# Kernel tuning notes

Measured on AMD Instinct MI355X. Metric: run time of the kernel, lower is better.

The kernel has to match this reference:

```python
import jax, jax.numpy as jnp
import numpy as np

DT = 0.1       # time separation between grid points (forward dt arg default)
UT = 0.1       # stationary-mode time constant
K_IN, K_OUT, K_STATE = 8, 4, 128
PRE_LEN, FWD_LEN, BATCH = 64, 128, 4096


def setup_inputs() -> dict:
    key = jax.random.key(0)
    ks = jax.random.split(key, 16)
    H = K_STATE
    s = 0.05  # small init keeps the 128-step integration numerically tame
    d = {}
    d['pre_x'] = jax.random.normal(ks[0], (PRE_LEN, BATCH, K_IN), jnp.float32)
    d['pre_y'] = jax.random.normal(ks[1], (PRE_LEN, BATCH, K_OUT), jnp.float32)
    d['forward_x'] = jax.random.normal(ks[2], (FWD_LEN, BATCH, K_IN), jnp.float32)
    # encoder nn.GRU (1 layer), torch gate order r,z,n
    d['W_ih'] = jax.random.normal(ks[3], (3 * H, K_IN + K_OUT), jnp.float32) * s
    d['W_hh'] = jax.random.normal(ks[4], (3 * H, H), jnp.float32) * s
    d['b_ih'] = jax.random.normal(ks[5], (3 * H,), jnp.float32) * s
    d['b_hh'] = jax.random.normal(ks[6], (3 * H,), jnp.float32) * s
    # expand_input: Linear(k_in, k_state) + Tanh
    d['W_e'] = jax.random.normal(ks[7], (H, K_IN), jnp.float32) * s
    d['b_e'] = jax.random.normal(ks[8], (H,), jnp.float32) * s
    # ODE GRU cell (BasicCell with net_type='GRU'): input size = k_state
    d['Wc_ih'] = jax.random.normal(ks[9], (3 * H, H), jnp.float32) * s
    d['Wc_hh'] = jax.random.normal(ks[10], (3 * H, H), jnp.float32) * s
    d['bc_ih'] = jax.random.normal(ks[11], (3 * H,), jnp.float32) * s
    d['bc_hh'] = jax.random.normal(ks[12], (3 * H,), jnp.float32) * s
    # fc: Linear(H, 2H, bias=False) -> Tanh -> Linear(2H, k_out, bias=False)
    d['W1'] = jax.random.normal(ks[13], (2 * H, H), jnp.float32) * s
    d['W2'] = jax.random.normal(ks[14], (K_OUT, 2 * H), jnp.float32) * s
    return d


def _gru_cell(x, h, Wi, Wh, bi, bh):
    gi = x @ Wi.T + bi
    gh = h @ Wh.T + bh
    ir, iz, inn = jnp.split(gi, 3, axis=-1)
    hr, hz, hn = jnp.split(gh, 3, axis=-1)
    r = jax.nn.sigmoid(ir + hr)
    z = jax.nn.sigmoid(iz + hz)
    n = jnp.tanh(inn + r * hn)
    return (1.0 - z) * n + z * h


def reference(pre_x, pre_y, forward_x, W_ih, W_hh, b_ih, b_hh, W_e, b_e,
              Wc_ih, Wc_hh, bc_ih, bc_hh, W1, W2):
    H = W_hh.shape[1]
    # ---- GRU encoder over [pre_x, pre_y], take final hidden state ----
    enc_in = jnp.concatenate([pre_x, pre_y], axis=2)  # [Tp, B, k_in+k_out]
    h0 = jnp.zeros((enc_in.shape[1], H), enc_in.dtype)

    def enc_step(h, x):
        return _gru_cell(x, h, W_ih, W_hh, b_ih, b_hh), None

    hn, _ = jax.lax.scan(enc_step, h0, enc_in)  # [B, H]

    # ---- natural cubic spline of the control input over the grid ----
    L = forward_x.shape[0]
    hs = DT
    ys = jnp.concatenate([pre_x[-1:], forward_x], axis=0)  # [L+1, B, k_in]
    rhs = 6.0 * (ys[:-2] - 2.0 * ys[1:-1] + ys[2:]) / (hs * hs)  # [L-1, ...]
    nin = L - 1
    A = 4.0 * jnp.eye(nin) + jnp.eye(nin, k=1) + jnp.eye(nin, k=-1)
    Minner = jnp.linalg.solve(A, rhs.reshape(nin, -1)).reshape(rhs.shape)
    zpad = jnp.zeros_like(ys[:1])
    M = jnp.concatenate([zpad, Minner, zpad], axis=0)  # 2nd derivs, [L+1,B,k_in]

    def u(t):
        i = jnp.clip(jnp.floor(t / hs).astype(jnp.int32), 0, L - 1)
        t0 = i.astype(ys.dtype) * hs
        a = (t0 + hs - t) / hs
        b = (t - t0) / hs
        yi, yi1 = jnp.take(ys, i, axis=0), jnp.take(ys, i + 1, axis=0)
        Mi, Mi1 = jnp.take(M, i, axis=0), jnp.take(M, i + 1, axis=0)
        return a * yi + b * yi1 + ((a ** 3 - a) * Mi + (b ** 3 - b) * Mi1) * (hs * hs) / 6.0

    # ---- ODE system: stationary GRU-cell dynamics ----
    def f(t, y):
        x = jnp.tanh(u(t) @ W_e.T + b_e)
        return (_gru_cell(x, y, Wc_ih, Wc_hh, bc_ih, bc_hh) - y) / UT

    # ---- fixed-grid RK4 (torchdiffeq method='rk4', one step per interval) ----
    def rk4(y, t0):
        k1 = f(t0, y)
        k2 = f(t0 + hs / 2, y + (hs / 2) * k1)
        k3 = f(t0 + hs / 2, y + (hs / 2) * k2)
        k4 = f(t0 + hs, y + hs * k3)
        yn = y + (hs / 6.0) * (k1 + 2 * k2 + 2 * k3 + k4)
        return yn, yn

    t_starts = jnp.arange(L, dtype=ys.dtype) * hs
    _, traj = jax.lax.scan(rk4, hn, t_starts)  # [L, B, H]

    # ---- output head: Linear -> Tanh -> Linear (no bias) ----
    return jnp.tanh(traj @ W1.T) @ W2.T  # [L, B, k_out]
```

## Files before the change

kernel.cpp:

```cpp
#include <hip/hip_runtime.h>
#include <math.h>

#define NB    4096
#define NH    128
#define NKIN  8
#define NKOUT 4
#define NTP   64
#define NL    128
#define BKIN  (NB*NKIN)
#define LOG2E 1.44269504088896340736f

typedef __attribute__((ext_vector_type(8))) short short8;
typedef __attribute__((ext_vector_type(4))) float f32x4;

#if __has_builtin(__builtin_amdgcn_exp2f)
#define EXP2F __builtin_amdgcn_exp2f
#else
#define EXP2F exp2f
#endif

__device__ __forceinline__ short f2bf(float f) {
    union { float f; unsigned u; } v; v.f = f;
    unsigned u = v.u;
    return (short)((u + 0x7fffu + ((u >> 16) & 1u)) >> 16);
}
__device__ __forceinline__ unsigned pkbf2(float a, float b) {
#if __has_builtin(__builtin_amdgcn_cvt_pk_bf16_f32)
    auto p = __builtin_amdgcn_cvt_pk_bf16_f32(a, b);
    unsigned q; __builtin_memcpy(&q, &p, 4); return q;
#else
    union { float f; unsigned u; } x, y; x.f = a; y.f = b;
    unsigned ua = (x.u + 0x7fffu + ((x.u >> 16) & 1u)) >> 16;
    unsigned ub = (y.u + 0x7fffu + ((y.u >> 16) & 1u)) & 0xffff0000u;
    return ua | ub;
#endif
}
__device__ __forceinline__ void st4(short* dst, const f32x4& v) {
    uint2 q; q.x = pkbf2(v[0], v[1]); q.y = pkbf2(v[2], v[3]);
    *(uint2*)dst = q;
}
__device__ __forceinline__ float tanh2(float a2) {
    return 1.0f - 2.0f*__builtin_amdgcn_rcpf(1.0f + EXP2F(a2));
}

__global__ void spline_um_kernel(const float* __restrict__ pre_x,
                                 const float* __restrict__ fx,
                                 float* __restrict__ UM)
{
    __shared__ float cp[128];
    if (threadIdx.x == 0) {
        float c = 0.f;
        for (int j = 1; j <= 127; ++j) { c = 1.0f/(4.0f - c); cp[j] = c; }
    }
    __syncthreads();
    int col = blockIdx.x*128 + threadIdx.x;
    const float r6 = 6.0f/(0.1f*0.1f);
    const float KK = 0.01f/16.0f;
    float y0 = pre_x[(size_t)(NTP-1)*BKIN + col];
    float y1 = fx[col];
    float d = 0.f;
    for (int j = 1; j <= 127; ++j) {
        float y2 = fx[(size_t)j*BKIN + col];
        float r  = r6*(y0 - 2.f*y1 + y2);
        d = (r - d)*cp[j];
        UM[(size_t)j*BKIN + col] = d;
        y0 = y1; y1 = y2;
    }
    float xn  = 0.f;
    float yj1 = fx[(size_t)127*BKIN + col];
    for (int j = 127; j >= 1; --j) {
        float dj = UM[(size_t)j*BKIN + col];
        float x  = dj - cp[j]*xn;
        float yj = fx[(size_t)(j-1)*BKIN + col];
        UM[(size_t)j*BKIN + col] = 0.5f*(yj + yj1) - KK*(x + xn);
        xn = x; yj1 = yj;
    }
    float ys0 = pre_x[(size_t)(NTP-1)*BKIN + col];
    UM[col] = 0.5f*(ys0 + yj1) - KK*xn;
}

__global__ void prep_frags(const float* __restrict__ W1, const float* __restrict__ W2,
                           short* __restrict__ w1f, short* __restrict__ w2f)
{
    int tid = threadIdx.x;
    for (int idx = tid; idx < 16*4*64*8; idx += 256) {
        int j = idx & 7, lane = (idx >> 3) & 63, kc = (idx >> 9) & 3, t = idx >> 11;
        int row = t*16 + (lane & 15);
        int k   = kc*32 + (lane >> 4)*8 + j;
        w1f[idx] = f2bf(2.0f*LOG2E*W1[row*NH + k]);
    }
    for (int idx = tid; idx < 8*64*8; idx += 256) {
        int j = idx & 7, lane = (idx >> 3) & 63, kc = idx >> 9;
        int m = lane & 15;
        int k = kc*32 + (lane >> 4)*8 + j;
        w2f[idx] = (m < NKOUT) ? f2bf(W2[m*2*NH + k]) : (short)0;
    }
}

__device__ __forceinline__ void gemmB(const short* bp, const short8 (&A)[3][4], f32x4 (&acc)[3])
{
    #pragma unroll
    for (int kc = 0; kc < 4; ++kc) {
        short8 b = *(const short8*)(bp + kc*32);
        #pragma unroll
        for (int g = 0; g < 3; ++g)
            acc[g] = __builtin_amdgcn_mfma_f32_16x16x32_bf16(A[g][kc], b, acc[g], 0, 0, 0);
    }
}
__device__ __forceinline__ void gateK(const f32x4 (&gi)[3], const f32x4 (&gh)[3],
                                      const f32x4& yin, f32x4& K)
{
    #pragma unroll
    for (int r = 0; r < 4; ++r) {
        float rg = __builtin_amdgcn_rcpf(1.0f + EXP2F(gi[0][r] + gh[0][r]));
        float zg = __builtin_amdgcn_rcpf(1.0f + EXP2F(gi[1][r] + gh[1][r]));
        float tg = tanh2(gi[2][r] + rg*gh[2][r]);
        K[r] = (1.0f - zg)*(tg - yin[r]);
    }
}

__global__ void __launch_bounds__(512, 2)
fused_kernel(const float* __restrict__ pre_x, const float* __restrict__ pre_y,
             const float* __restrict__ fx,
             const float* __restrict__ W_ih, const float* __restrict__ W_hh,
             const float* __restrict__ b_ih, const float* __restrict__ b_hh,
             const float* __restrict__ W_e,  const float* __restrict__ b_e,
             const float* __restrict__ Wc_ih,const float* __restrict__ Wc_hh,
             const float* __restrict__ bc_ih,const float* __restrict__ bc_hh,
             const float* __restrict__ UM,   const short* __restrict__ w1f,
             const short* __restrict__ w2f,  float* __restrict__ out)
{
    __shared__ __align__(16) short yTa[16*136];
    __shared__ __align__(16) short yTb[16*136];
    __shared__ __align__(16) short E1 [16*136];
    __shared__ __align__(16) short xmT[16*136];
    __shared__ __align__(16) short x1T[16*136];
    __shared__ __align__(16) short UMb[16*40];
    __shared__ __align__(16) short U1b[16*40];
    __shared__ __align__(16) short oT [16*264];

    const int tid  = threadIdx.x;
    const int w    = tid >> 6;
    const int lane = tid & 63;
    const int quad = lane >> 4;
    const int m    = lane & 15;
    const int hq   = w*16 + quad*4;
    const int b0   = blockIdx.x * 16;
    const f32x4 z4 = {0.f, 0.f, 0.f, 0.f};
    const float scg[3] = {-LOG2E, -LOG2E, 2.0f*LOG2E};

    for (int i = tid; i < 16*136; i += 512) yTa[i] = 0;
    for (int i = tid; i < 16*40;  i += 512) { UMb[i] = 0; U1b[i] = 0; }

    f32x4 y = z4;

    {
        short8 Ehh[3][4];
        #pragma unroll
        for (int g = 0; g < 3; ++g)
            #pragma unroll
            for (int c = 0; c < 4; ++c) {
                const float* ph = W_hh + (size_t)(g*NH + w*16 + m)*NH + c*32 + quad*8;
                short8 fh;
                #pragma unroll
                for (int j = 0; j < 8; ++j) fh[j] = f2bf(scg[g]*ph[j]);
                Ehh[g][c] = fh;
            }
        short8 Eih[3];
        #pragma unroll
        for (int g = 0; g < 3; ++g) {
            short8 f1;
            #pragma unroll
            for (int j = 0; j < 8; ++j) {
                int k = quad*8 + j;
                f1[j] = (k < 12) ? f2bf(scg[g]*W_ih[(size_t)(g*NH + w*16 + m)*12 + k]) : (short)0;
            }
            Eih[g] = f1;
        }
        f32x4 erz4, ezz4, egn4, ein4;
        #pragma unroll
        for (int r = 0; r < 4; ++r) {
            int h = hq + r;
            erz4[r] = -LOG2E*(b_ih[h]      + b_hh[h]);
            ezz4[r] = -LOG2E*(b_ih[NH + h] + b_hh[NH + h]);
            egn4[r] = 2.0f*LOG2E*b_hh[2*NH + h];
            ein4[r] = 2.0f*LOG2E*b_ih[2*NH + h];
        }
        const int eb = tid / 12, ek = tid - eb*12;
        float encv = 0.f;
        if (tid < 192) {
            float e0 = (ek < NKIN) ? pre_x[((size_t)0*NB + b0 + eb)*NKIN + ek]
                                   : pre_y[((size_t)0*NB + b0 + eb)*NKOUT + (ek - NKIN)];
            UMb[eb*40 + ek] = f2bf(e0);
            encv = (ek < NKIN) ? pre_x[((size_t)1*NB + b0 + eb)*NKIN + ek]
                               : pre_y[((size_t)1*NB + b0 + eb)*NKOUT + (ek - NKIN)];
        }
        __syncthreads();
        for (int t = 0; t < NTP; ++t) {
            float evn = 0.f;
            if (tid < 192) {
                int tn = (t + 2 < NTP) ? t + 2 : NTP - 1;
                evn = (ek < NKIN) ? pre_x[((size_t)tn*NB + b0 + eb)*NKIN + ek]
                                  : pre_y[((size_t)tn*NB + b0 + eb)*NKOUT + (ek - NKIN)];
            }
            const short* bin_buf  = (t & 1) ? U1b : UMb;
            short*       bout_buf = (t & 1) ? UMb : U1b;
            const short* sin_buf  = (t & 1) ? yTb : yTa;
            short*       sout_buf = (t & 1) ? yTa : yTb;
            f32x4 gi[3] = {z4, z4, ein4};
            {
                short8 b = *(const short8*)(bin_buf + m*40 + quad*8);
                #pragma unroll
                for (int g = 0; g < 3; ++g)
                    gi[g] = __builtin_amdgcn_mfma_f32_16x16x32_bf16(Eih[g], b, gi[g], 0, 0, 0);
            }
            f32x4 gh[3] = {erz4, ezz4, egn4};
            gemmB(sin_buf + m*136 + quad*8, Ehh, gh);
            f32x4 K;
            gateK(gi, gh, y, K);
            #pragma unroll
            for (int r = 0; r < 4; ++r) y[r] += K[r];
            st4(sout_buf + m*136 + hq, y);
            if (tid < 192) { bout_buf[eb*40 + ek] = f2bf(encv); encv = evn; }
            __syncthreads();
        }
    }

    short8 Ahh[3][4], Aih[3][4];
    #pragma unroll
    for (int g = 0; g < 3; ++g)
        #pragma unroll
        for (int c = 0; c < 4; ++c) {
            const float* ph = Wc_hh + (size_t)(g*NH + w*16 + m)*NH + c*32 + quad*8;
            const float* pi = Wc_ih + (size_t)(g*NH + w*16 + m)*NH + c*32 + quad*8;
            short8 fh, fi;
            #pragma unroll
            for (int j = 0; j < 8; ++j) { fh[j] = f2bf(scg[g]*ph[j]); fi[j] = f2bf(scg[g]*pi[j]); }
            Ahh[g][c] = fh; Aih[g][c] = fi;
        }
    short8 Aexp;
    #pragma unroll
    for (int j = 0; j < 8; ++j) {
        int k = quad*8 + j;
        Aexp[j] = (k < NKIN) ? f2bf(2.0f*LOG2E*W_e[(w*16 + m)*NKIN + k]) : (short)0;
    }
    short8 A1f[2][4];
    #pragma unroll
    for (int kc = 0; kc < 4; ++kc) {
        A1f[0][kc] = *(const short8*)(w1f + (size_t)(((w    )*4 + kc)*64 + lane)*8);
        A1f[1][kc] = *(const short8*)(w1f + (size_t)(((w + 8)*4 + kc)*64 + lane)*8);
    }
    f32x4 brz4, bzz4, bgn4, bin4, be4;
    #pragma unroll
    for (int r = 0; r < 4; ++r) {
        int h = hq + r;
        brz4[r] = -LOG2E*(bc_ih[h]      + bc_hh[h]);
        bzz4[r] = -LOG2E*(bc_ih[NH + h] + bc_hh[NH + h]);
        bgn4[r] = 2.0f*LOG2E*bc_hh[2*NH + h];
        bin4[r] = 2.0f*LOG2E*bc_ih[2*NH + h];
        be4[r]  = 2.0f*LOG2E*b_e[h];
    }

    const int sb = tid >> 3, sk = tid & 7;
    const size_t scol = (size_t)(b0 + sb)*NKIN + sk;
    if (tid < 128) {
        short* bb = (tid & 64) ? U1b : UMb;
        int rr = (tid >> 2) & 15, cc = 8 + (tid & 3);
        bb[rr*40 + cc] = 0;
    }
    if (tid < 128) UMb[sb*40 + sk] = f2bf(pre_x[(size_t)(NTP-1)*BKIN + scol]);
    __syncthreads();
    {
        short8 b = *(const short8*)(UMb + m*40 + quad*8);
        f32x4 c0 = be4;
        c0 = __builtin_amdgcn_mfma_f32_16x16x32_bf16(Aexp, b, c0, 0, 0, 0);
        f32x4 xv;
        #pragma unroll
        for (int r = 0; r < 4; ++r) xv[r] = tanh2(c0[r]);
        st4(xmT + m*136 + hq, xv);
    }
    __syncthreads();
    f32x4 gi0[3] = {z4, z4, bin4};
    gemmB(xmT + m*136 + quad*8, Aih, gi0);
    if (tid < 128) { UMb[sb*40 + sk] = f2bf(UM[scol]); U1b[sb*40 + sk] = f2bf(fx[scol]); }
    __syncthreads();
    {
        short8 bm = *(const short8*)(UMb + m*40 + quad*8);
        short8 b1 = *(const short8*)(U1b + m*40 + quad*8);
        f32x4 cm = be4, c1 = be4;
        cm = __builtin_amdgcn_mfma_f32_16x16x32_bf16(Aexp, bm, cm, 0, 0, 0);
        c1 = __builtin_amdgcn_mfma_f32_16x16x32_bf16(Aexp, b1, c1, 0, 0, 0);
        f32x4 xm, x1;
        #pragma unroll
        for (int r = 0; r < 4; ++r) { xm[r] = tanh2(cm[r]); x1[r] = tanh2(c1[r]); }
        st4(xmT + m*136 + hq, xm);
        st4(x1T + m*136 + hq, x1);
    }
    __syncthreads();
    f32x4 gim[3] = {z4, z4, bin4}, gi1[3] = {z4, z4, bin4};
    gemmB(xmT + m*136 + quad*8, Aih, gim);
    gemmB(x1T + m*136 + quad*8, Aih, gi1);
    float fxv = 0.f, umv = 0.f;
    if (tid < 128) { fxv = fx[(size_t)BKIN + scol]; umv = UM[(size_t)BKIN + scol]; }

    for (int st = 0; st < NL; ++st) {
        f32x4 gh[3] = {brz4, bzz4, bgn4};
        gemmB(yTa + m*136 + quad*8, Ahh, gh);
        if (st > 0) {
            f32x4 o0 = z4, o1 = z4;
            #pragma unroll
            for (int kc = 0; kc < 4; ++kc) {
                short8 b = *(const short8*)(yTa + m*136 + quad*8 + kc*32);
                o0 = __builtin_amdgcn_mfma_f32_16x16x32_bf16(A1f[0][kc], b, o0, 0, 0, 0);
                o1 = __builtin_amdgcn_mfma_f32_16x16x32_bf16(A1f[1][kc], b, o1, 0, 0, 0);
            }
            f32x4 t0, t1;
            #pragma unroll
            for (int r = 0; r < 4; ++r) { t0[r] = tanh2(o0[r]); t1[r] = tanh2(o1[r]); }
            st4(oT + m*264 + w*16     + quad*4, t0);
            st4(oT + m*264 + (w+8)*16 + quad*4, t1);
        }
        f32x4 K, Ks, ye;
        gateK(gi0, gh, y, K);
        #pragma unroll
        for (int r = 0; r < 4; ++r) { Ks[r] = K[r]; ye[r] = y[r] + 0.5f*K[r]; }
        st4(yTb + m*136 + hq, ye);
        __syncthreads();
        float fxn = 0.f, umn = 0.f;
        if (tid < 128) {
            int sn = (st + 2 < NL) ? st + 2 : NL - 1;
            fxn = fx[(size_t)sn*BKIN + scol];
            umn = UM[(size_t)sn*BKIN + scol];
        }
        if (st > 0 && w == ((st-1) & 7)) {
            short8 a2f[8];
            #pragma unroll
            for (int kc = 0; kc < 8; ++kc)
                a2f[kc] = *(const short8*)(w2f + (size_t)(kc*64 + lane)*8);
            f32x4 oc = z4;
            #pragma unroll
            for (int kc = 0; kc < 8; ++kc) {
                short8 b = *(const short8*)(oT + m*264 + kc*32 + quad*8);
                oc = __builtin_amdgcn_mfma_f32_16x16x32_bf16(a2f[kc], b, oc, 0, 0, 0);
            }
            if (quad == 0)
                *(f32x4*)(out + ((size_t)(st-1)*NB + b0 + m)*NKOUT) = oc;
        }
        if (tid < 128) { UMb[sb*40 + sk] = f2bf(umv); U1b[sb*40 + sk] = f2bf(fxv); }
        gh[0] = brz4; gh[1] = bzz4; gh[2] = bgn4;
        gemmB(yTb + m*136 + quad*8, Ahh, gh);
        gateK(gim, gh, ye, K);
        #pragma unroll
        for (int r = 0; r < 4; ++r) { Ks[r] += 2.f*K[r]; ye[r] = y[r] + 0.5f*K[r]; }
        st4(E1 + m*136 + hq, ye);
        fxv = fxn; umv = umn;
        __syncthreads();
        gh[0] = brz4; gh[1] = bzz4; gh[2] = bgn4;
        gemmB(E1 + m*136 + quad*8, Ahh, gh);
        {
            short8 bm = *(const short8*)(UMb + m*40 + quad*8);
            short8 b1 = *(const short8*)(U1b + m*40 + quad*8);
            f32x4 cm = be4, c1 = be4;
            cm = __builtin_amdgcn_mfma_f32_16x16x32_bf16(Aexp, bm, cm, 0, 0, 0);
            c1 = __builtin_amdgcn_mfma_f32_16x16x32_bf16(Aexp, b1, c1, 0, 0, 0);
            f32x4 xm, x1;
            #pragma unroll
            for (int r = 0; r < 4; ++r) { xm[r] = tanh2(cm[r]); x1[r] = tanh2(c1[r]); }
            st4(xmT + m*136 + hq, xm);
            st4(x1T + m*136 + hq, x1);
        }
        gateK(gim, gh, ye, K);
        #pragma unroll
        for (int r = 0; r < 4; ++r) { Ks[r] += 2.f*K[r]; ye[r] = y[r] + K[r]; }
        st4(yTb + m*136 + hq, ye);
        __syncthreads();
        gh[0] = brz4; gh[1] = bzz4; gh[2] = bgn4;
        gemmB(yTb + m*136 + quad*8, Ahh, gh);
        gateK(gi1, gh, ye, K);
        #pragma unroll
        for (int r = 0; r < 4; ++r) y[r] += (1.0f/6.0f)*(Ks[r] + K[r]);
        st4(yTa + m*136 + hq, y);
        gi0[0] = gi1[0]; gi0[1] = gi1[1]; gi0[2] = gi1[2];
        gim[0] = z4; gim[1] = z4; gim[2] = bin4;
        gi1[0] = z4; gi1[1] = z4; gi1[2] = bin4;
        gemmB(xmT + m*136 + quad*8, Aih, gim);
        gemmB(x1T + m*136 + quad*8, Aih, gi1);
        __syncthreads();
    }

    {
        f32x4 o0 = z4, o1 = z4;
        #pragma unroll
        for (int kc = 0; kc < 4; ++kc) {
            short8 b = *(const short8*)(yTa + m*136 + quad*8 + kc*32);
            o0 = __builtin_amdgcn_mfma_f32_16x16x32_bf16(A1f[0][kc], b, o0, 0, 0, 0);
            o1 = __builtin_amdgcn_mfma_f32_16x16x32_bf16(A1f[1][kc], b, o1, 0, 0, 0);
        }
        f32x4 t0, t1;
        #pragma unroll
        for (int r = 0; r < 4; ++r) { t0[r] = tanh2(o0[r]); t1[r] = tanh2(o1[r]); }
        st4(oT + m*264 + w*16     + quad*4, t0);
        st4(oT + m*264 + (w+8)*16 + quad*4, t1);
        short8 a2f[8];
        if (w == 7) {
            #pragma unroll
            for (int kc = 0; kc < 8; ++kc)
                a2f[kc] = *(const short8*)(w2f + (size_t)(kc*64 + lane)*8);
        }
        __syncthreads();
        if (w == 7) {
            f32x4 oc = z4;
            #pragma unroll
            for (int kc = 0; kc < 8; ++kc) {
                short8 b = *(const short8*)(oT + m*264 + kc*32 + quad*8);
                oc = __builtin_amdgcn_mfma_f32_16x16x32_bf16(a2f[kc], b, oc, 0, 0, 0);
            }
            if (quad == 0)
                *(f32x4*)(out + ((size_t)(NL-1)*NB + b0 + m)*NKOUT) = oc;
        }
    }
}

extern "C" void kernel_launch(void* const* d_in, const int* in_sizes, int n_in,
                              void* d_out, int out_size, void* d_ws, size_t ws_size,
                              hipStream_t stream)
{
    const float* pre_x = (const float*)d_in[0];
    const float* pre_y = (const float*)d_in[1];
    const float* fx    = (const float*)d_in[2];
    const float* W_ih  = (const float*)d_in[3];
    const float* W_hh  = (const float*)d_in[4];
    const float* b_ih  = (const float*)d_in[5];
    const float* b_hh  = (const float*)d_in[6];
    const float* W_e   = (const float*)d_in[7];
    const float* b_e   = (const float*)d_in[8];
    const float* Wc_ih = (const float*)d_in[9];
    const float* Wc_hh = (const float*)d_in[10];
    const float* bc_ih = (const float*)d_in[11];
    const float* bc_hh = (const float*)d_in[12];
    const float* W1    = (const float*)d_in[13];
    const float* W2    = (const float*)d_in[14];
    float* out = (float*)d_out;

    float* UM  = (float*)d_ws;
    short* w1f = (short*)((char*)d_ws + (size_t)NL*NB*NKIN*4);
    short* w2f = w1f + 16*4*64*8;

    prep_frags<<<dim3(1), dim3(256), 0, stream>>>(W1, W2, w1f, w2f);
    spline_um_kernel<<<dim3((NB*NKIN)/128), dim3(128), 0, stream>>>(pre_x, fx, UM);
    fused_kernel<<<dim3(NB/16), dim3(512), 0, stream>>>(
        pre_x, pre_y, fx, W_ih, W_hh, b_ih, b_hh, W_e, b_e,
        Wc_ih, Wc_hh, bc_ih, bc_hh, UM, w1f, w2f, out);
}
```

Baseline: 843.2 us.

## Reschedule RK4 stage loop to overlap input projections and output head with stage GEMMs

Reorders the per-step RK4 loop so the input-projection GEMMs for the midpoint and endpoint stages run just before their use, and the output-head MFMAs and the W2 stage are moved into different sync phases to fill idle slots. It also reuses the loaded state fragments for both the recurrent GEMM and the output head, flips the sign of the z-gate scaling so (1-z) comes straight from a reciprocal, vectorizes the gate math, and spreads the staging loads across all waves instead of the first few. The aim is to shorten the serial chain between barriers and cut redundant LDS reads, at the cost of more live registers per thread.

```diff
diff --git a/kernel.cpp b/kernel.cpp
--- a/kernel.cpp
+++ b/kernel.cpp
@@ -39,8 +39,17 @@
     uint2 q; q.x = pkbf2(v[0], v[1]); q.y = pkbf2(v[2], v[3]);
     *(uint2*)dst = q;
 }
-__device__ __forceinline__ float tanh2(float a2) {
-    return 1.0f - 2.0f*__builtin_amdgcn_rcpf(1.0f + EXP2F(a2));
+__device__ __forceinline__ f32x4 exp24(f32x4 a) {
+    f32x4 r;
+    #pragma unroll
+    for (int i = 0; i < 4; ++i) r[i] = EXP2F(a[i]);
+    return r;
+}
+__device__ __forceinline__ f32x4 rcp4(f32x4 a) {
+    f32x4 r;
+    #pragma unroll
+    for (int i = 0; i < 4; ++i) r[i] = __builtin_amdgcn_rcpf(a[i]);
+    return r;
 }
 
 __global__ void spline_um_kernel(const float* __restrict__ pre_x,
@@ -97,26 +106,28 @@
     }
 }
 
-__device__ __forceinline__ void gemmB(const short* bp, const short8 (&A)[3][4], f32x4 (&acc)[3])
-{
-    #pragma unroll
-    for (int kc = 0; kc < 4; ++kc) {
-        short8 b = *(const short8*)(bp + kc*32);
+__device__ __forceinline__ void ld4(const short* bp, short8 (&bf)[4]) {
+    #pragma unroll
+    for (int kc = 0; kc < 4; ++kc) bf[kc] = *(const short8*)(bp + kc*32);
+}
+__device__ __forceinline__ void gemmR(const short8 (&bf)[4], const short8 (&A)[3][4],
+                                      f32x4 (&acc)[3]) {
+    #pragma unroll
+    for (int kc = 0; kc < 4; ++kc)
         #pragma unroll
         for (int g = 0; g < 3; ++g)
-            acc[g] = __builtin_amdgcn_mfma_f32_16x16x32_bf16(A[g][kc], b, acc[g], 0, 0, 0);
-    }
+            acc[g] = __builtin_amdgcn_mfma_f32_16x16x32_bf16(A[g][kc], bf[kc], acc[g], 0, 0, 0);
+}
+__device__ __forceinline__ void gemmB(const short* bp, const short8 (&A)[3][4], f32x4 (&acc)[3]) {
+    short8 bf[4]; ld4(bp, bf); gemmR(bf, A, acc);
 }
 __device__ __forceinline__ void gateK(const f32x4 (&gi)[3], const f32x4 (&gh)[3],
                                       const f32x4& yin, f32x4& K)
 {
-    #pragma unroll
-    for (int r = 0; r < 4; ++r) {
-        float rg = __builtin_amdgcn_rcpf(1.0f + EXP2F(gi[0][r] + gh[0][r]));
-        float zg = __builtin_amdgcn_rcpf(1.0f + EXP2F(gi[1][r] + gh[1][r]));
-        float tg = tanh2(gi[2][r] + rg*gh[2][r]);
-        K[r] = (1.0f - zg)*(tg - yin[r]);
-    }
+    f32x4 rg = rcp4(exp24(gi[0] + gh[0]) + 1.0f);
+    f32x4 zc = rcp4(exp24(gi[1] + gh[1]) + 1.0f);
+    f32x4 tg = 1.0f - 2.0f*rcp4(exp24(gi[2] + rg*gh[2]) + 1.0f);
+    K = zc*(tg - yin);
 }
 
 __global__ void __launch_bounds__(512, 2)
@@ -147,7 +158,7 @@
     const int hq   = w*16 + quad*4;
     const int b0   = blockIdx.x * 16;
     const f32x4 z4 = {0.f, 0.f, 0.f, 0.f};
-    const float scg[3] = {-LOG2E, -LOG2E, 2.0f*LOG2E};
+    const float scg[3] = {-LOG2E, LOG2E, 2.0f*LOG2E};
 
     for (int i = tid; i < 16*136; i += 512) yTa[i] = 0;
     for (int i = tid; i < 16*40;  i += 512) { UMb[i] = 0; U1b[i] = 0; }
@@ -182,13 +193,15 @@
         for (int r = 0; r < 4; ++r) {
             int h = hq + r;
             erz4[r] = -LOG2E*(b_ih[h]      + b_hh[h]);
-            ezz4[r] = -LOG2E*(b_ih[NH + h] + b_hh[NH + h]);
+            ezz4[r] =  LOG2E*(b_ih[NH + h] + b_hh[NH + h]);
             egn4[r] = 2.0f*LOG2E*b_hh[2*NH + h];
             ein4[r] = 2.0f*LOG2E*b_ih[2*NH + h];
         }
-        const int eb = tid / 12, ek = tid - eb*12;
+        const int eidx = w*24 + lane;
+        const int eb = eidx/12, ek = eidx - 12*eb;
+        const bool estg = (lane < 24);
         float encv = 0.f;
-        if (tid < 192) {
+        if (estg) {
             float e0 = (ek < NKIN) ? pre_x[((size_t)0*NB + b0 + eb)*NKIN + ek]
                                    : pre_y[((size_t)0*NB + b0 + eb)*NKOUT + (ek - NKIN)];
             UMb[eb*40 + ek] = f2bf(e0);
@@ -198,7 +211,7 @@
         __syncthreads();
         for (int t = 0; t < NTP; ++t) {
             float evn = 0.f;
-            if (tid < 192) {
+            if (estg) {
                 int tn = (t + 2 < NTP) ? t + 2 : NTP - 1;
                 evn = (ek < NKIN) ? pre_x[((size_t)tn*NB + b0 + eb)*NKIN + ek]
                                   : pre_y[((size_t)tn*NB + b0 + eb)*NKOUT + (ek - NKIN)];
@@ -218,10 +231,9 @@
             gemmB(sin_buf + m*136 + quad*8, Ehh, gh);
             f32x4 K;
             gateK(gi, gh, y, K);
-            #pragma unroll
-            for (int r = 0; r < 4; ++r) y[r] += K[r];
+            y += K;
             st4(sout_buf + m*136 + hq, y);
-            if (tid < 192) { bout_buf[eb*40 + ek] = f2bf(encv); encv = evn; }
+            if (estg) { bout_buf[eb*40 + ek] = f2bf(encv); encv = evn; }
             __syncthreads();
         }
     }
@@ -255,34 +267,32 @@
     for (int r = 0; r < 4; ++r) {
         int h = hq + r;
         brz4[r] = -LOG2E*(bc_ih[h]      + bc_hh[h]);
-        bzz4[r] = -LOG2E*(bc_ih[NH + h] + bc_hh[NH + h]);
+        bzz4[r] =  LOG2E*(bc_ih[NH + h] + bc_hh[NH + h]);
         bgn4[r] = 2.0f*LOG2E*bc_hh[2*NH + h];
         bin4[r] = 2.0f*LOG2E*bc_ih[2*NH + h];
         be4[r]  = 2.0f*LOG2E*b_e[h];
     }
 
-    const int sb = tid >> 3, sk = tid & 7;
+    const bool stg = (lane < 16);
+    const int sb = w*2 + (lane >> 3), sk = lane & 7;
     const size_t scol = (size_t)(b0 + sb)*NKIN + sk;
-    if (tid < 128) {
-        short* bb = (tid & 64) ? U1b : UMb;
-        int rr = (tid >> 2) & 15, cc = 8 + (tid & 3);
-        bb[rr*40 + cc] = 0;
-    }
-    if (tid < 128) UMb[sb*40 + sk] = f2bf(pre_x[(size_t)(NTP-1)*BKIN + scol]);
+    if (stg) {
+        UMb[sb*40 + 8 + (lane & 3)] = 0;
+        U1b[sb*40 + 8 + (lane & 3)] = 0;
+        UMb[sb*40 + sk] = f2bf(pre_x[(size_t)(NTP-1)*BKIN + scol]);
+    }
     __syncthreads();
     {
         short8 b = *(const short8*)(UMb + m*40 + quad*8);
         f32x4 c0 = be4;
         c0 = __builtin_amdgcn_mfma_f32_16x16x32_bf16(Aexp, b, c0, 0, 0, 0);
-        f32x4 xv;
-        #pragma unroll
-        for (int r = 0; r < 4; ++r) xv[r] = tanh2(c0[r]);
+        f32x4 xv = 1.0f - 2.0f*rcp4(exp24(c0) + 1.0f);
         st4(xmT + m*136 + hq, xv);
     }
     __syncthreads();
     f32x4 gi0[3] = {z4, z4, bin4};
     gemmB(xmT + m*136 + quad*8, Aih, gi0);
-    if (tid < 128) { UMb[sb*40 + sk] = f2bf(UM[scol]); U1b[sb*40 + sk] = f2bf(fx[scol]); }
+    if (stg) { UMb[sb*40 + sk] = f2bf(UM[scol]); U1b[sb*40 + sk] = f2bf(fx[scol]); }
     __syncthreads();
     {
         short8 bm = *(const short8*)(UMb + m*40 + quad*8);
@@ -290,115 +300,107 @@
         f32x4 cm = be4, c1 = be4;
         cm = __builtin_amdgcn_mfma_f32_16x16x32_bf16(Aexp, bm, cm, 0, 0, 0);
         c1 = __builtin_amdgcn_mfma_f32_16x16x32_bf16(Aexp, b1, c1, 0, 0, 0);
-        f32x4 xm, x1;
-        #pragma unroll
-        for (int r = 0; r < 4; ++r) { xm[r] = tanh2(cm[r]); x1[r] = tanh2(c1[r]); }
+        f32x4 xm = 1.0f - 2.0f*rcp4(exp24(cm) + 1.0f);
+        f32x4 x1 = 1.0f - 2.0f*rcp4(exp24(c1) + 1.0f);
         st4(xmT + m*136 + hq, xm);
         st4(x1T + m*136 + hq, x1);
     }
+    float fxv = 0.f, umv = 0.f;
+    if (stg) { fxv = fx[(size_t)BKIN + scol]; umv = UM[(size_t)BKIN + scol]; }
     __syncthreads();
-    f32x4 gim[3] = {z4, z4, bin4}, gi1[3] = {z4, z4, bin4};
-    gemmB(xmT + m*136 + quad*8, Aih, gim);
-    gemmB(x1T + m*136 + quad*8, Aih, gi1);
-    float fxv = 0.f, umv = 0.f;
-    if (tid < 128) { fxv = fx[(size_t)BKIN + scol]; umv = UM[(size_t)BKIN + scol]; }
 
     for (int st = 0; st < NL; ++st) {
+        short8 byf[4];
+        ld4(yTa + m*136 + quad*8, byf);
         f32x4 gh[3] = {brz4, bzz4, bgn4};
-        gemmB(yTa + m*136 + quad*8, Ahh, gh);
+        gemmR(byf, Ahh, gh);
+        f32x4 gim[3] = {z4, z4, bin4};
+        gemmB(xmT + m*136 + quad*8, Aih, gim);
+        f32x4 K, Ks, ye;
+        gateK(gi0, gh, y, K);
+        Ks = K; ye = y + 0.5f*K;
+        st4(yTb + m*136 + hq, ye);
+        __syncthreads();
+        if (stg) { UMb[sb*40 + sk] = f2bf(umv); U1b[sb*40 + sk] = f2bf(fxv); }
+        gh[0] = brz4; gh[1] = bzz4; gh[2] = bgn4;
+        gemmB(yTb + m*136 + quad*8, Ahh, gh);
         if (st > 0) {
             f32x4 o0 = z4, o1 = z4;
             #pragma unroll
             for (int kc = 0; kc < 4; ++kc) {
-                short8 b = *(const short8*)(yTa + m*136 + quad*8 + kc*32);
-                o0 = __builtin_amdgcn_mfma_f32_16x16x32_bf16(A1f[0][kc], b, o0, 0, 0, 0);
-                o1 = __builtin_amdgcn_mfma_f32_16x16x32_bf16(A1f[1][kc], b, o1, 0, 0, 0);
-            }
-            f32x4 t0, t1;
-            #pragma unroll
-            for (int r = 0; r < 4; ++r) { t0[r] = tanh2(o0[r]); t1[r] = tanh2(o1[r]); }
+                o0 = __builtin_amdgcn_mfma_f32_16x16x32_bf16(A1f[0][kc], byf[kc], o0, 0, 0, 0);
+                o1 = __builtin_amdgcn_mfma_f32_16x16x32_bf16(A1f[1][kc], byf[kc], o1, 0, 0, 0);
+            }
+            f32x4 t0 = 1.0f - 2.0f*rcp4(exp24(o0) + 1.0f);
+            f32x4 t1 = 1.0f - 2.0f*rcp4(exp24(o1) + 1.0f);
             st4(oT + m*264 + w*16     + quad*4, t0);
             st4(oT + m*264 + (w+8)*16 + quad*4, t1);
         }
-        f32x4 K, Ks, ye;
-        gateK(gi0, gh, y, K);
-        #pragma unroll
-        for (int r = 0; r < 4; ++r) { Ks[r] = K[r]; ye[r] = y[r] + 0.5f*K[r]; }
+        gateK(gim, gh, ye, K);
+        Ks += 2.0f*K; ye = y + 0.5f*K;
+        st4(E1 + m*136 + hq, ye);
+        __syncthreads();
+        if (stg) {
+            int sn = (st + 2 < NL) ? st + 2 : NL - 1;
+            fxv = fx[(size_t)sn*BKIN + scol];
+            umv = UM[(size_t)sn*BKIN + scol];
+        }
+        gh[0] = brz4; gh[1] = bzz4; gh[2] = bgn4;
+        gemmB(E1 + m*136 + quad*8, Ahh, gh);
+        f32x4 gi1[3] = {z4, z4, bin4};
+        gemmB(x1T + m*136 + quad*8, Aih, gi1);
+        gateK(gim, gh, ye, K);
+        Ks += 2.0f*K; ye = y + K;
         st4(yTb + m*136 + hq, ye);
         __syncthreads();
-        float fxn = 0.f, umn = 0.f;
-        if (tid < 128) {
-            int sn = (st + 2 < NL) ? st + 2 : NL - 1;
-            fxn = fx[(size_t)sn*BKIN + scol];
-            umn = UM[(size_t)sn*BKIN + scol];
-        }
-        if (st > 0 && w == ((st-1) & 7)) {
-            short8 a2f[8];
+        short8 a2f[8];
+        const bool s2w = (st > 0) && (w == ((st-1) & 7));
+        if (s2w) {
             #pragma unroll
             for (int kc = 0; kc < 8; ++kc)
                 a2f[kc] = *(const short8*)(w2f + (size_t)(kc*64 + lane)*8);
-            f32x4 oc = z4;
-            #pragma unroll
-            for (int kc = 0; kc < 8; ++kc) {
-                short8 b = *(const short8*)(oT + m*264 + kc*32 + quad*8);
-                oc = __builtin_amdgcn_mfma_f32_16x16x32_bf16(a2f[kc], b, oc, 0, 0, 0);
-            }
-            if (quad == 0)
-                *(f32x4*)(out + ((size_t)(st-1)*NB + b0 + m)*NKOUT) = oc;
-        }
-        if (tid < 128) { UMb[sb*40 + sk] = f2bf(umv); U1b[sb*40 + sk] = f2bf(fxv); }
+        }
         gh[0] = brz4; gh[1] = bzz4; gh[2] = bgn4;
         gemmB(yTb + m*136 + quad*8, Ahh, gh);
-        gateK(gim, gh, ye, K);
-        #pragma unroll
-        for (int r = 0; r < 4; ++r) { Ks[r] += 2.f*K[r]; ye[r] = y[r] + 0.5f*K[r]; }
-        st4(E1 + m*136 + hq, ye);
-        fxv = fxn; umv = umn;
-        __syncthreads();
-        gh[0] = brz4; gh[1] = bzz4; gh[2] = bgn4;
-        gemmB(E1 + m*136 + quad*8, Ahh, gh);
         {
             short8 bm = *(const short8*)(UMb + m*40 + quad*8);
             short8 b1 = *(const short8*)(U1b + m*40 + quad*8);
             f32x4 cm = be4, c1 = be4;
             cm = __builtin_amdgcn_mfma_f32_16x16x32_bf16(Aexp, bm, cm, 0, 0, 0);
             c1 = __builtin_amdgcn_mfma_f32_16x16x32_bf16(Aexp, b1, c1, 0, 0, 0);
-            f32x4 xm, x1;
-            #pragma unroll
-            for (int r = 0; r < 4; ++r) { xm[r] = tanh2(cm[r]); x1[r] = tanh2(c1[r]); }
+            f32x4 xm = 1.0f - 2.0f*rcp4(exp24(cm) + 1.0f);
+            f32x4 x1 = 1.0f - 2.0f*rcp4(exp24(c1) + 1.0f);
             st4(xmT + m*136 + hq, xm);
             st4(x1T + m*136 + hq, x1);
         }
-        gateK(gim, gh, ye, K);
-        #pragma unroll
-        for (int r = 0; r < 4; ++r) { Ks[r] += 2.f*K[r]; ye[r] = y[r] + K[r]; }
-        st4(yTb + m*136 + hq, ye);
-        __syncthreads();
-        gh[0] = brz4; gh[1] = bzz4; gh[2] = bgn4;
-        gemmB(yTb + m*136 + quad*8, Ahh, gh);
+        if (s2w) {
+            f32x4 oc = z4;
+            #pragma unroll
+            for (int kc = 0; kc < 8; ++kc) {
+                short8 b = *(const short8*)(oT + m*264 + kc*32 + quad*8);
+                oc = __builtin_amdgcn_mfma_f32_16x16x32_bf16(a2f[kc], b, oc, 0, 0, 0);
+            }
+            if (quad == 0)
+                *(f32x4*)(out + ((size_t)(st-1)*NB + b0 + m)*NKOUT) = oc;
+        }
         gateK(gi1, gh, ye, K);
-        #pragma unroll
-        for (int r = 0; r < 4; ++r) y[r] += (1.0f/6.0f)*(Ks[r] + K[r]);
+        y += (1.0f/6.0f)*(Ks + K);
         st4(yTa + m*136 + hq, y);
         gi0[0] = gi1[0]; gi0[1] = gi1[1]; gi0[2] = gi1[2];
-        gim[0] = z4; gim[1] = z4; gim[2] = bin4;
-        gi1[0] = z4; gi1[1] = z4; gi1[2] = bin4;
-        gemmB(xmT + m*136 + quad*8, Aih, gim);
-        gemmB(x1T + m*136 + quad*8, Aih, gi1);
         __syncthreads();
     }
 
     {
+        short8 byf[4];
+        ld4(yTa + m*136 + quad*8, byf);
         f32x4 o0 = z4, o1 = z4;
         #pragma unroll
         for (int kc = 0; kc < 4; ++kc) {
-            short8 b = *(const short8*)(yTa + m*136 + quad*8 + kc*32);
-            o0 = __builtin_amdgcn_mfma_f32_16x16x32_bf16(A1f[0][kc], b, o0, 0, 0, 0);
-            o1 = __builtin_amdgcn_mfma_f32_16x16x32_bf16(A1f[1][kc], b, o1, 0, 0, 0);
-        }
-        f32x4 t0, t1;
-        #pragma unroll
-        for (int r = 0; r < 4; ++r) { t0[r] = tanh2(o0[r]); t1[r] = tanh2(o1[r]); }
+            o0 = __builtin_amdgcn_mfma_f32_16x16x32_bf16(A1f[0][kc], byf[kc], o0, 0, 0, 0);
+            o1 = __builtin_amdgcn_mfma_f32_16x16x32_bf16(A1f[1][kc], byf[kc], o1, 0, 0, 0);
+        }
+        f32x4 t0 = 1.0f - 2.0f*rcp4(exp24(o0) + 1.0f);
+        f32x4 t1 = 1.0f - 2.0f*rcp4(exp24(o1) + 1.0f);
         st4(oT + m*264 + w*16     + quad*4, t0);
         st4(oT + m*264 + (w+8)*16 + quad*4, t1);
         short8 a2f[8];
```

Result: no change. 840.4 us (-0.3%).
